# Kernel tuning notes

Measured on AMD Instinct MI355X. Metric: run time of the kernel, lower is better.

Reference implementation:

```python
import jax, jax.numpy as jnp
import numpy as np

B, S, D = 2, 2048, 1024
H, DH = 16, 64
INNER = H * DH  # 1024
FF = 4 * D
WINDOW = 128
EPS = 1e-5
SCALE = DH ** -0.5


def setup_inputs() -> dict:
    key = jax.random.key(0)
    ks = jax.random.split(key, 8)
    s = lambda fan_in: 1.0 / np.sqrt(fan_in)
    return {
        "x": jax.random.normal(ks[0], (B, S, D), dtype=jnp.float32),
        "ln1_g": jnp.ones((D,), jnp.float32),
        "ln1_b": jnp.zeros((D,), jnp.float32),
        "w_qkv": jax.random.uniform(ks[1], (3 * INNER, D), jnp.float32, -s(D), s(D)),
        "w_out": jax.random.uniform(ks[2], (D, INNER), jnp.float32, -s(INNER), s(INNER)),
        "b_out": jnp.zeros((D,), jnp.float32),
        "ln2_g": jnp.ones((D,), jnp.float32),
        "ln2_b": jnp.zeros((D,), jnp.float32),
        "w_ff1": jax.random.uniform(ks[3], (FF, D), jnp.float32, -s(D), s(D)),
        "b_ff1": jnp.zeros((FF,), jnp.float32),
        "w_ff2": jax.random.uniform(ks[4], (D, FF), jnp.float32, -s(FF), s(FF)),
        "b_ff2": jnp.zeros((D,), jnp.float32),
    }


def _layernorm(x, g, b):
    mu = jnp.mean(x, axis=-1, keepdims=True)
    var = jnp.mean(jnp.square(x - mu), axis=-1, keepdims=True)
    return (x - mu) * jax.lax.rsqrt(var + EPS) * g + b


def reference(x, ln1_g, ln1_b, w_qkv, w_out, b_out, ln2_g, ln2_b, w_ff1, b_ff1, w_ff2, b_ff2):
    # --- attention block ---
    residual = x
    h = _layernorm(x, ln1_g, ln1_b)
    qkv = h @ w_qkv.T                             # [B, S, 3*INNER]
    q, k, v = jnp.split(qkv, 3, axis=-1)
    reshape_heads = lambda t: t.reshape(B, S, H, DH).transpose(0, 2, 1, 3)  # [B,H,S,DH]
    q, k, v = map(reshape_heads, (q, k, v))
    q = q * SCALE
    scores = jnp.einsum("bhqd,bhkd->bhqk", q, k)  # dense [B,H,S,S]
    # local sparse pattern: attend iff |i-j| <= window_size
    idx = jnp.arange(S)
    local_mask = jnp.abs(idx[:, None] - idx[None, :]) <= WINDOW  # [S,S] bool
    scores = jnp.where(local_mask[None, None], scores, -jnp.inf)
    attn = jax.nn.softmax(scores, axis=-1)
    attn = jnp.nan_to_num(attn, nan=0.0)
    out = jnp.einsum("bhqk,bhkd->bhqd", attn, v)  # [B,H,S,DH]
    out = out.transpose(0, 2, 1, 3).reshape(B, S, INNER)
    out = out @ w_out.T + b_out                   # dropout inactive (eval)
    x = residual + out
    # --- FFN block ---
    residual = x
    h = _layernorm(x, ln2_g, ln2_b)
    h = jax.nn.gelu(h @ w_ff1.T + b_ff1, approximate=False)
    h = h @ w_ff2.T + b_ff2
    return residual + h
```

## Files before the change

### kernel.cpp

```cpp
#include <hip/hip_runtime.h>
#include <stdint.h>

#define SEQ    2048
#define NB     2
#define DMODEL 1024
#define NHEAD  16
#define HDIM   64
#define FFDIM  4096
#define WIN    128
#define MTOK   (NB*SEQ)

typedef short short8 __attribute__((ext_vector_type(8)));
typedef float f32x4  __attribute__((ext_vector_type(4)));

__device__ __forceinline__ float bf2f(uint16_t h){ return __uint_as_float(((uint32_t)h) << 16); }
__device__ __forceinline__ uint16_t f2bf(float f){
  uint32_t u = __float_as_uint(f);
  u += 0x7fffu + ((u >> 16) & 1u);
  return (uint16_t)(u >> 16);
}

__device__ __forceinline__ float gelu_f(float v){
  float u = 0.7978845608028654f * v * (1.0f + 0.044715f * v * v);
  u = fminf(fmaxf(u, -10.0f), 10.0f);
  const float e = __expf(2.0f * u);
  const float th = (e - 1.0f) / (e + 1.0f);
  return 0.5f * v * (1.0f + th);
}

__device__ __forceinline__ void gl_lds16(const void* g, void* l) {
  __builtin_amdgcn_global_load_lds((const __attribute__((address_space(1))) void*)g,
                                   (__attribute__((address_space(3))) void*)l, 16, 0, 0);
}

__device__ __forceinline__ void BAR() {
  asm volatile("" ::: "memory");
  __builtin_amdgcn_s_barrier();
  asm volatile("" ::: "memory");
}

__global__ __launch_bounds__(256) void cvtln_kernel(
    const float* __restrict__ s0, const float* __restrict__ s1,
    const float* __restrict__ s2, const float* __restrict__ s3,
    uint16_t* __restrict__ d0, uint16_t* __restrict__ d1,
    uint16_t* __restrict__ d2, uint16_t* __restrict__ d3,
    const float* __restrict__ x, const float* __restrict__ g,
    const float* __restrict__ b, uint16_t* __restrict__ y)
{
  __shared__ float red[8];
  const int t = threadIdx.x;
  if (blockIdx.x < 12288) {
    size_t i = (size_t)blockIdx.x * 256 + t;
    const float* s; uint16_t* d; size_t off;
    if      (i <  768*1024) { s = s0; d = d0; off = i; }
    else if (i < 1024*1024) { s = s1; d = d1; off = i -  768*1024; }
    else if (i < 2048*1024) { s = s2; d = d2; off = i - 1024*1024; }
    else                    { s = s3; d = d3; off = i - 2048*1024; }
    const float4 v = ((const float4*)s)[off];
    uint2 o;
    o.x = (uint32_t)f2bf(v.x) | ((uint32_t)f2bf(v.y) << 16);
    o.y = (uint32_t)f2bf(v.z) | ((uint32_t)f2bf(v.w) << 16);
    ((uint2*)d)[off] = o;
  } else {
    const int row = blockIdx.x - 12288;
    const float4 v = ((const float4*)(x + (size_t)row * DMODEL))[t];
    float s1 = v.x + v.y + v.z + v.w;
    float s2 = v.x*v.x + v.y*v.y + v.z*v.z + v.w*v.w;
    #pragma unroll
    for (int off = 32; off; off >>= 1) { s1 += __shfl_xor(s1, off, 64); s2 += __shfl_xor(s2, off, 64); }
    const int w = t >> 6;
    if ((t & 63) == 0) { red[w] = s1; red[4+w] = s2; }
    __syncthreads();
    s1 = red[0]+red[1]+red[2]+red[3];
    s2 = red[4]+red[5]+red[6]+red[7];
    const float mu = s1 * (1.0f/DMODEL);
    const float var = s2 * (1.0f/DMODEL) - mu*mu;
    const float rs = rsqrtf(var + 1e-5f);
    const float4 gv = ((const float4*)g)[t];
    const float4 bv = ((const float4*)b)[t];
    uint2 o;
    o.x = (uint32_t)f2bf((v.x-mu)*rs*gv.x + bv.x) | ((uint32_t)f2bf((v.y-mu)*rs*gv.y + bv.y) << 16);
    o.y = (uint32_t)f2bf((v.z-mu)*rs*gv.z + bv.z) | ((uint32_t)f2bf((v.w-mu)*rs*gv.w + bv.w) << 16);
    ((uint2*)(y + (size_t)row * DMODEL))[t] = o;
  }
}

__global__ __launch_bounds__(256) void ln_kernel(const float* __restrict__ x,
                                                 const float* __restrict__ g,
                                                 const float* __restrict__ b,
                                                 uint16_t* __restrict__ y)
{
  const int row = blockIdx.x;
  const int t = threadIdx.x;
  const float4 v = ((const float4*)(x + (size_t)row * DMODEL))[t];
  float s1 = v.x + v.y + v.z + v.w;
  float s2 = v.x*v.x + v.y*v.y + v.z*v.z + v.w*v.w;
  #pragma unroll
  for (int off = 32; off; off >>= 1) { s1 += __shfl_xor(s1, off, 64); s2 += __shfl_xor(s2, off, 64); }
  __shared__ float red[8];
  const int w = t >> 6;
  if ((t & 63) == 0) { red[w] = s1; red[4+w] = s2; }
  __syncthreads();
  s1 = red[0]+red[1]+red[2]+red[3];
  s2 = red[4]+red[5]+red[6]+red[7];
  const float mu = s1 * (1.0f/DMODEL);
  const float var = s2 * (1.0f/DMODEL) - mu*mu;
  const float rs = rsqrtf(var + 1e-5f);
  const float4 gv = ((const float4*)g)[t];
  const float4 bv = ((const float4*)b)[t];
  uint2 o;
  o.x = (uint32_t)f2bf((v.x-mu)*rs*gv.x + bv.x) | ((uint32_t)f2bf((v.y-mu)*rs*gv.y + bv.y) << 16);
  o.y = (uint32_t)f2bf((v.z-mu)*rs*gv.z + bv.z) | ((uint32_t)f2bf((v.w-mu)*rs*gv.w + bv.w) << 16);
  ((uint2*)(y + (size_t)row * DMODEL))[t] = o;
}

template<int EPI>
__global__ __launch_bounds__(512, 2) void gemm256(
    const uint16_t* __restrict__ A, const uint16_t* __restrict__ Bm,
    const float* __restrict__ bias, uint16_t* __restrict__ C,
    int M, int N, int K)
{
  __shared__ __align__(16) uint16_t L[4 * 16384];
  const int t = threadIdx.x;
  const int l = t & 63;
  const int w = t >> 6;
  const int wm = w >> 2, wn = w & 3;
  const int row0 = blockIdx.y * 256, col0 = blockIdx.x * 256;
  const int mrow = l & 15, kq = l >> 4;
  const int nt = K >> 5;

  f32x4 acc[8][4];
  #pragma unroll
  for (int i = 0; i < 8; ++i)
    #pragma unroll
    for (int j = 0; j < 4; ++j)
      #pragma unroll
      for (int e = 0; e < 4; ++e) acc[i][j][e] = 0.0f;

  const int sr = t >> 2;
  const int kl = (t & 3) ^ ((t >> 3) & 3);
  const uint16_t* aG = A  + (size_t)(row0 + sr) * K + kl * 8;
  const uint16_t* bG = Bm + (size_t)(col0 + sr) * K + kl * 8;
  char* const lds = (char*)L;
  const int soff = t * 16;

  #define STAGE_A(tt_) { char* d_ = lds + ((tt_) & 3) * 32768 + soff; \
      gl_lds16(aG + (tt_) * 32, d_); \
      gl_lds16(aG + (size_t)128 * K + (tt_) * 32, d_ + 8192); }
  #define STAGE_B(tt_) { char* d_ = lds + ((tt_) & 3) * 32768 + 16384 + soff; \
      gl_lds16(bG + (tt_) * 32, d_); \
      gl_lds16(bG + (size_t)128 * K + (tt_) * 32, d_ + 8192); }

  STAGE_A(0); STAGE_B(0);
  STAGE_A(1); STAGE_B(1);
  STAGE_A(2); STAGE_B(2);
  asm volatile("s_waitcnt vmcnt(8)" ::: "memory");
  BAR();

  const int cphys = (kq ^ ((mrow >> 1) & 3)) << 4;

  for (int tt = 0; tt < nt; ++tt) {
    char* const bufA = lds + (tt & 3) * 32768;
    char* const bufB = bufA + 16384;
    short8 bf[4], af[4];
    #pragma unroll
    for (int ni = 0; ni < 4; ++ni)
      bf[ni] = *(const short8*)(bufB + (wn*64 + ni*16 + mrow) * 64 + cphys);
    #pragma unroll
    for (int mi = 0; mi < 4; ++mi)
      af[mi] = *(const short8*)(bufA + (wm*128 + mi*16 + mrow) * 64 + cphys);
    if (tt + 3 < nt) STAGE_A(tt + 3);
    BAR();
    __builtin_amdgcn_s_setprio(1);
    #pragma unroll
    for (int mi = 0; mi < 4; ++mi)
      #pragma unroll
      for (int ni = 0; ni < 4; ++ni)
        acc[mi][ni] = __builtin_amdgcn_mfma_f32_16x16x32_bf16(af[mi], bf[ni], acc[mi][ni], 0, 0, 0);
    __builtin_amdgcn_s_setprio(0);
    BAR();
    #pragma unroll
    for (int mi = 0; mi < 4; ++mi)
      af[mi] = *(const short8*)(bufA + (wm*128 + (mi+4)*16 + mrow) * 64 + cphys);
    if (tt + 3 < nt) {
      STAGE_B(tt + 3);
      asm volatile("s_waitcnt vmcnt(8)" ::: "memory");
    } else if (tt + 3 == nt) {
      asm volatile("s_waitcnt vmcnt(4)" ::: "memory");
    } else if (tt + 2 == nt) {
      asm volatile("s_waitcnt vmcnt(0)" ::: "memory");
    }
    BAR();
    __builtin_amdgcn_s_setprio(1);
    #pragma unroll
    for (int mi = 0; mi < 4; ++mi)
      #pragma unroll
      for (int ni = 0; ni < 4; ++ni)
        acc[mi+4][ni] = __builtin_amdgcn_mfma_f32_16x16x32_bf16(af[mi], bf[ni], acc[mi+4][ni], 0, 0, 0);
    __builtin_amdgcn_s_setprio(0);
    BAR();
  }
  #undef STAGE_A
  #undef STAGE_B

  const int crow = kq * 4;
  float bv[4];
  #pragma unroll
  for (int ni = 0; ni < 4; ++ni)
    bv[ni] = (EPI != 0) ? bias[col0 + wn*64 + ni*16 + mrow] : 0.0f;
  #pragma unroll
  for (int mi = 0; mi < 8; ++mi) {
    #pragma unroll
    for (int r = 0; r < 4; ++r) {
      const int row = row0 + wm*128 + mi*16 + crow + r;
      uint16_t* Cr = C + (size_t)row * N + col0 + wn*64 + mrow;
      #pragma unroll
      for (int ni = 0; ni < 4; ++ni) {
        float v = acc[mi][ni][r] + bv[ni];
        if (EPI == 2) v = gelu_f(v);
        Cr[ni*16] = f2bf(v);
      }
    }
  }
}

__global__ __launch_bounds__(256) void gemm64(
    const uint16_t* __restrict__ A, const uint16_t* __restrict__ Bm,
    const float* __restrict__ bias, const float* __restrict__ res,
    float* __restrict__ out, int M, int N, int K)
{
  __shared__ __align__(16) uint16_t As[64*64];
  __shared__ __align__(16) uint16_t Bs[64*64];
  const int t = threadIdx.x;
  const int l = t & 63;
  const int w = t >> 6;
  const int row0 = blockIdx.y * 64;
  const int col0 = blockIdx.x * 64;
  const int wm = (w >> 1) * 32, wn = (w & 1) * 32;

  f32x4 acc[2][2];
  #pragma unroll
  for (int i = 0; i < 2; ++i)
    #pragma unroll
    for (int j = 0; j < 2; ++j)
      #pragma unroll
      for (int e = 0; e < 4; ++e) acc[i][j][e] = 0.0f;

  const int sr8 = t >> 3;
  const int sg  = (t & 7) ^ (sr8 & 7);
  const uint16_t* aG = A  + (size_t)(row0 + sr8) * K + sg * 8;
  const uint16_t* bG = Bm + (size_t)(col0 + sr8) * K + sg * 8;
  char* aL = (char*)As + t * 16;
  char* bL = (char*)Bs + t * 16;
  const int mrow = l & 15;
  const int kq = l >> 4;

  for (int k0 = 0; k0 < K; k0 += 64) {
    gl_lds16(aG + k0,                    aL);
    gl_lds16(aG + k0 + (size_t)32 * K,   aL + 4096);
    gl_lds16(bG + k0,                    bL);
    gl_lds16(bG + k0 + (size_t)32 * K,   bL + 4096);
    __syncthreads();
    #pragma unroll
    for (int ks = 0; ks < 2; ++ks) {
      const int pa = ((ks*4 + kq) ^ (mrow & 7)) * 16;
      short8 af[2], bfr[2];
      #pragma unroll
      for (int mi = 0; mi < 2; ++mi)
        af[mi] = *(const short8*)((const char*)As + (wm + mi*16 + mrow) * 128 + pa);
      #pragma unroll
      for (int ni = 0; ni < 2; ++ni)
        bfr[ni] = *(const short8*)((const char*)Bs + (wn + ni*16 + mrow) * 128 + pa);
      #pragma unroll
      for (int mi = 0; mi < 2; ++mi)
        #pragma unroll
        for (int ni = 0; ni < 2; ++ni)
          acc[mi][ni] = __builtin_amdgcn_mfma_f32_16x16x32_bf16(af[mi], bfr[ni], acc[mi][ni], 0, 0, 0);
    }
    __syncthreads();
  }

  const int crow = (l >> 4) * 4;
  float bv[2];
  #pragma unroll
  for (int ni = 0; ni < 2; ++ni)
    bv[ni] = bias[col0 + wn + ni*16 + mrow];
  #pragma unroll
  for (int mi = 0; mi < 2; ++mi)
    #pragma unroll
    for (int r = 0; r < 4; ++r) {
      const int row = row0 + wm + mi*16 + crow + r;
      #pragma unroll
      for (int ni = 0; ni < 2; ++ni) {
        const int col = col0 + wn + ni*16 + mrow;
        out[(size_t)row * N + col] = acc[mi][ni][r] + bv[ni] + res[(size_t)row * N + col];
      }
    }
}

#define TQ    32
#define NKT   18
#define NKP   (NKT*16)
#define KSTR  72
#define PSTR  296

__global__ __launch_bounds__(256) void attn_kernel(const uint16_t* __restrict__ qkv,
                                                   uint16_t* __restrict__ out)
{
  __shared__ uint16_t Qs[TQ * KSTR];
  __shared__ uint16_t Ps[TQ * PSTR];
  __shared__ uint16_t KV[NKP * KSTR];
  const int t = threadIdx.x, l = t & 63, w = t >> 6;
  const int b = blockIdx.z, hh = blockIdx.y, q0 = blockIdx.x * TQ;
  const int k0 = (q0 - WIN > 0) ? (q0 - WIN) : 0;
  const int kend_ = q0 + TQ + WIN;
  const int kend = (kend_ < SEQ) ? kend_ : SEQ;
  const int nk = kend - k0;

  {
    const int r = t >> 3, gg = t & 7;
    const uint4 qv = *(const uint4*)(qkv + (size_t)(b*SEQ + q0 + r) * 3072 + hh*64 + gg*8);
    *(uint4*)((char*)Qs + r*(KSTR*2) + gg*16) = qv;
    for (int j = r; j < NKP; j += 32) {
      uint4 kv; kv.x = 0; kv.y = 0; kv.z = 0; kv.w = 0;
      if (j < nk)
        kv = *(const uint4*)(qkv + (size_t)(b*SEQ + k0 + j) * 3072 + 1024 + hh*64 + gg*8);
      *(uint4*)((char*)KV + j*(KSTR*2) + gg*16) = kv;
    }
  }
  __syncthreads();

  if (w < 2) {
    const int rb = w * 16;
    const int mrow = l & 15, q4 = l >> 4;
    const short8 aq0 = *(const short8*)((const char*)Qs + (rb + mrow)*(KSTR*2) + q4*16);
    const short8 aq1 = *(const short8*)((const char*)Qs + (rb + mrow)*(KSTR*2) + 64 + q4*16);
    f32x4 cacc[NKT];
    #pragma unroll
    for (int ct = 0; ct < NKT; ++ct) {
      f32x4 c; c[0]=0.f; c[1]=0.f; c[2]=0.f; c[3]=0.f;
      const short8 b0 = *(const short8*)((const char*)KV + (ct*16 + mrow)*(KSTR*2) + q4*16);
      const short8 b1 = *(const short8*)((const char*)KV + (ct*16 + mrow)*(KSTR*2) + 64 + q4*16);
      c = __builtin_amdgcn_mfma_f32_16x16x32_bf16(aq0, b0, c, 0, 0, 0);
      c = __builtin_amdgcn_mfma_f32_16x16x32_bf16(aq1, b1, c, 0, 0, 0);
      cacc[ct] = c;
    }
    #pragma unroll
    for (int r = 0; r < 4; ++r) {
      const int iq = q0 + rb + q4*4 + r;
      float m = -1e30f;
      #pragma unroll
      for (int ct = 0; ct < NKT; ++ct) {
        const int jj = ct*16 + mrow;
        const int j = k0 + jj;
        const bool ok = (jj < nk) && (j >= iq - WIN) && (j <= iq + WIN);
        const float s = ok ? cacc[ct][r] * 0.125f : -1e30f;
        cacc[ct][r] = s;
        m = fmaxf(m, s);
      }
      m = fmaxf(m, __shfl_xor(m, 1, 64));
      m = fmaxf(m, __shfl_xor(m, 2, 64));
      m = fmaxf(m, __shfl_xor(m, 4, 64));
      m = fmaxf(m, __shfl_xor(m, 8, 64));
      float s = 0.f;
      #pragma unroll
      for (int ct = 0; ct < NKT; ++ct) {
        const float e = __expf(cacc[ct][r] - m);
        cacc[ct][r] = e;
        s += e;
      }
      s += __shfl_xor(s, 1, 64);
      s += __shfl_xor(s, 2, 64);
      s += __shfl_xor(s, 4, 64);
      s += __shfl_xor(s, 8, 64);
      const float rinv = 1.0f / s;
      #pragma unroll
      for (int ct = 0; ct < NKT; ++ct)
        Ps[(rb + q4*4 + r) * PSTR + ct*16 + mrow] = f2bf(cacc[ct][r] * rinv);
    }
  }
  __syncthreads();

  {
    uint16_t* Vt = KV;
    const int gg = t & 7;
    for (int j = t >> 3; j < NKP; j += 32) {
      if (j < nk) {
        const uint4 v = *(const uint4*)(qkv + (size_t)(b*SEQ + k0 + j) * 3072 + 2048 + hh*64 + gg*8);
        uint16_t e[8] = { (uint16_t)(v.x & 0xffff), (uint16_t)(v.x >> 16),
                          (uint16_t)(v.y & 0xffff), (uint16_t)(v.y >> 16),
                          (uint16_t)(v.z & 0xffff), (uint16_t)(v.z >> 16),
                          (uint16_t)(v.w & 0xffff), (uint16_t)(v.w >> 16) };
        #pragma unroll
        for (int dd = 0; dd < 8; ++dd) Vt[(gg*8 + dd) * PSTR + j] = e[dd];
      } else {
        #pragma unroll
        for (int dd = 0; dd < 8; ++dd) Vt[(gg*8 + dd) * PSTR + j] = 0;
      }
    }
  }
  __syncthreads();

  {
    const uint16_t* Vt = KV;
    const int mrow = l & 15, q4 = l >> 4;
    const int rt = w & 1, dt0 = (w >> 1) * 2;
    f32x4 o0, o1;
    #pragma unroll
    for (int e = 0; e < 4; ++e) { o0[e] = 0.f; o1[e] = 0.f; }
    #pragma unroll
    for (int ks = 0; ks < 9; ++ks) {
      const short8 a  = *(const short8*)((const char*)Ps + (rt*16 + mrow)*(PSTR*2) + ks*64 + q4*16);
      const short8 v0 = *(const short8*)((const char*)Vt + ((dt0  )*16 + mrow)*(PSTR*2) + ks*64 + q4*16);
      const short8 v1 = *(const short8*)((const char*)Vt + ((dt0+1)*16 + mrow)*(PSTR*2) + ks*64 + q4*16);
      o0 = __builtin_amdgcn_mfma_f32_16x16x32_bf16(a, v0, o0, 0, 0, 0);
      o1 = __builtin_amdgcn_mfma_f32_16x16x32_bf16(a, v1, o1, 0, 0, 0);
    }
    #pragma unroll
    for (int r = 0; r < 4; ++r) {
      const int iq = q0 + rt*16 + q4*4 + r;
      const size_t rowoff = (size_t)(b*SEQ + iq) * DMODEL + hh*64;
      out[rowoff + (dt0  )*16 + mrow] = f2bf(o0[r]);
      out[rowoff + (dt0+1)*16 + mrow] = f2bf(o1[r]);
    }
  }
}

extern "C" void kernel_launch(void* const* d_in, const int* in_sizes, int n_in,
                              void* d_out, int out_size, void* d_ws, size_t ws_size,
                              hipStream_t stream)
{
  const float* x    = (const float*)d_in[0];
  const float* ln1g = (const float*)d_in[1];
  const float* ln1b = (const float*)d_in[2];
  const float* wqkv = (const float*)d_in[3];
  const float* wout = (const float*)d_in[4];
  const float* bout = (const float*)d_in[5];
  const float* ln2g = (const float*)d_in[6];
  const float* ln2b = (const float*)d_in[7];
  const float* wff1 = (const float*)d_in[8];
  const float* bff1 = (const float*)d_in[9];
  const float* wff2 = (const float*)d_in[10];
  const float* bff2 = (const float*)d_in[11];
  float* out = (float*)d_out;

  char* ws = (char*)d_ws;
  const size_t MB = (size_t)1 << 20;
  uint16_t* Wqkv = (uint16_t*)(ws);
  uint16_t* Wout = (uint16_t*)(ws +  6*MB);
  uint16_t* Wff1 = (uint16_t*)(ws +  8*MB);
  uint16_t* Wff2 = (uint16_t*)(ws + 16*MB);
  uint16_t* QKV  = (uint16_t*)(ws + 24*MB);
  uint16_t* H1   = (uint16_t*)(ws + 48*MB);
  uint16_t* AT   = H1;
  float*    X2f  = (float*)   (ws + 56*MB);
  uint16_t* H2   = (uint16_t*)(ws + 72*MB);
  uint16_t* FF1  = (uint16_t*)(ws + 24*MB);

  cvtln_kernel<<<16384, 256, 0, stream>>>(wqkv, wout, wff1, wff2,
                                          Wqkv, Wout, Wff1, Wff2,
                                          x, ln1g, ln1b, H1);
  gemm256<0><<<dim3(3072/256, MTOK/256), 512, 0, stream>>>(H1, Wqkv, nullptr, QKV, MTOK, 3072, DMODEL);
  attn_kernel<<<dim3(SEQ/TQ, NHEAD, NB), 256, 0, stream>>>(QKV, AT);
  gemm64<<<dim3(DMODEL/64, MTOK/64), 256, 0, stream>>>(AT, Wout, bout, x, X2f, MTOK, DMODEL, DMODEL);
  ln_kernel<<<MTOK, 256, 0, stream>>>(X2f, ln2g, ln2b, H2);
  gemm256<2><<<dim3(FFDIM/256, MTOK/256), 512, 0, stream>>>(H2, Wff1, bff1, FF1, MTOK, FFDIM, DMODEL);
  gemm64<<<dim3(DMODEL/64, MTOK/64), 256, 0, stream>>>(FF1, Wff2, bff2, X2f, out, MTOK, DMODEL, FFDIM);
}
```

Before: 331.7 us.

## Replace gemm64 with pipelined 128x128 GEMM and overlap V staging in attention

Replaces the 64x64 single-buffered residual GEMM with a 128x128, 512-thread kernel. It uses a 4-deep LDS ring of direct global-to-LDS loads, explicit vmcnt waits, and s_setprio around the MFMA bursts, to hide load latency and cut per-tile overhead. The attention kernel now prefetches V into registers while Q/K are staged, and moves the V-transpose onto the two idle waves so it runs alongside the softmax. It also swizzles the transposed V layout to reduce LDS bank conflicts. The costs are extra registers, 128KB of LDS per block for the GEMM (which limits occupancy), and a subtle wait-count schedule.

After: 314.8 us. 5.1% less time.

```diff
diff --git a/kernel.cpp b/kernel.cpp
--- a/kernel.cpp
+++ b/kernel.cpp
@@ -224,77 +224,116 @@
   }
 }
 
-__global__ __launch_bounds__(256) void gemm64(
+__global__ __launch_bounds__(512, 2) void gemm128r(
     const uint16_t* __restrict__ A, const uint16_t* __restrict__ Bm,
     const float* __restrict__ bias, const float* __restrict__ res,
     float* __restrict__ out, int M, int N, int K)
 {
-  __shared__ __align__(16) uint16_t As[64*64];
-  __shared__ __align__(16) uint16_t Bs[64*64];
+  __shared__ __align__(16) uint16_t L[4 * 16384];
   const int t = threadIdx.x;
   const int l = t & 63;
   const int w = t >> 6;
-  const int row0 = blockIdx.y * 64;
-  const int col0 = blockIdx.x * 64;
-  const int wm = (w >> 1) * 32, wn = (w & 1) * 32;
-
-  f32x4 acc[2][2];
-  #pragma unroll
-  for (int i = 0; i < 2; ++i)
+  const int wm = w >> 2, wn = w & 3;
+  const int row0 = blockIdx.x * 128, col0 = blockIdx.y * 128;
+  const int mrow = l & 15, kq = l >> 4;
+  const int nt = K >> 6;
+
+  f32x4 acc[4][2];
+  #pragma unroll
+  for (int i = 0; i < 4; ++i)
     #pragma unroll
     for (int j = 0; j < 2; ++j)
       #pragma unroll
       for (int e = 0; e < 4; ++e) acc[i][j][e] = 0.0f;
 
-  const int sr8 = t >> 3;
-  const int sg  = (t & 7) ^ (sr8 & 7);
-  const uint16_t* aG = A  + (size_t)(row0 + sr8) * K + sg * 8;
-  const uint16_t* bG = Bm + (size_t)(col0 + sr8) * K + sg * 8;
-  char* aL = (char*)As + t * 16;
-  char* bL = (char*)Bs + t * 16;
-  const int mrow = l & 15;
-  const int kq = l >> 4;
-
-  for (int k0 = 0; k0 < K; k0 += 64) {
-    gl_lds16(aG + k0,                    aL);
-    gl_lds16(aG + k0 + (size_t)32 * K,   aL + 4096);
-    gl_lds16(bG + k0,                    bL);
-    gl_lds16(bG + k0 + (size_t)32 * K,   bL + 4096);
-    __syncthreads();
-    #pragma unroll
-    for (int ks = 0; ks < 2; ++ks) {
-      const int pa = ((ks*4 + kq) ^ (mrow & 7)) * 16;
-      short8 af[2], bfr[2];
-      #pragma unroll
-      for (int mi = 0; mi < 2; ++mi)
-        af[mi] = *(const short8*)((const char*)As + (wm + mi*16 + mrow) * 128 + pa);
+  const int sr = t >> 3;
+  const int kl = (t & 7) ^ (sr & 7);
+  const uint16_t* aG = A  + (size_t)(row0 + sr) * K + kl * 8;
+  const uint16_t* bG = Bm + (size_t)(col0 + sr) * K + kl * 8;
+  char* const lds = (char*)L;
+  const int soff = t * 16;
+
+  #define STAGE_A(tt_) { char* d_ = lds + ((tt_) & 3) * 32768 + soff; \
+      gl_lds16(aG + (tt_) * 64, d_); \
+      gl_lds16(aG + (size_t)64 * K + (tt_) * 64, d_ + 8192); }
+  #define STAGE_B(tt_) { char* d_ = lds + ((tt_) & 3) * 32768 + 16384 + soff; \
+      gl_lds16(bG + (tt_) * 64, d_); \
+      gl_lds16(bG + (size_t)64 * K + (tt_) * 64, d_ + 8192); }
+
+  STAGE_A(0); STAGE_B(0);
+  STAGE_A(1); STAGE_B(1);
+  STAGE_A(2); STAGE_B(2);
+  asm volatile("s_waitcnt vmcnt(8)" ::: "memory");
+  BAR();
+
+  for (int tt = 0; tt < nt; ++tt) {
+    char* const bufA = lds + (tt & 3) * 32768;
+    char* const bufB = bufA + 16384;
+    {
+      const int pa = (kq ^ (mrow & 7)) * 16;
+      short8 af[4], bf[2];
       #pragma unroll
       for (int ni = 0; ni < 2; ++ni)
-        bfr[ni] = *(const short8*)((const char*)Bs + (wn + ni*16 + mrow) * 128 + pa);
-      #pragma unroll
-      for (int mi = 0; mi < 2; ++mi)
+        bf[ni] = *(const short8*)(bufB + (wn*32 + ni*16 + mrow) * 128 + pa);
+      #pragma unroll
+      for (int mi = 0; mi < 4; ++mi)
+        af[mi] = *(const short8*)(bufA + (wm*64 + mi*16 + mrow) * 128 + pa);
+      if (tt + 3 < nt) STAGE_A(tt + 3);
+      BAR();
+      __builtin_amdgcn_s_setprio(1);
+      #pragma unroll
+      for (int mi = 0; mi < 4; ++mi)
         #pragma unroll
         for (int ni = 0; ni < 2; ++ni)
-          acc[mi][ni] = __builtin_amdgcn_mfma_f32_16x16x32_bf16(af[mi], bfr[ni], acc[mi][ni], 0, 0, 0);
-    }
-    __syncthreads();
-  }
-
-  const int crow = (l >> 4) * 4;
+          acc[mi][ni] = __builtin_amdgcn_mfma_f32_16x16x32_bf16(af[mi], bf[ni], acc[mi][ni], 0, 0, 0);
+      __builtin_amdgcn_s_setprio(0);
+      BAR();
+    }
+    {
+      const int pa = ((4 + kq) ^ (mrow & 7)) * 16;
+      short8 af[4], bf[2];
+      #pragma unroll
+      for (int ni = 0; ni < 2; ++ni)
+        bf[ni] = *(const short8*)(bufB + (wn*32 + ni*16 + mrow) * 128 + pa);
+      #pragma unroll
+      for (int mi = 0; mi < 4; ++mi)
+        af[mi] = *(const short8*)(bufA + (wm*64 + mi*16 + mrow) * 128 + pa);
+      if (tt + 3 < nt) {
+        STAGE_B(tt + 3);
+        asm volatile("s_waitcnt vmcnt(8)" ::: "memory");
+      } else if (tt + 3 == nt) {
+        asm volatile("s_waitcnt vmcnt(4)" ::: "memory");
+      } else if (tt + 2 == nt) {
+        asm volatile("s_waitcnt vmcnt(0)" ::: "memory");
+      }
+      BAR();
+      __builtin_amdgcn_s_setprio(1);
+      #pragma unroll
+      for (int mi = 0; mi < 4; ++mi)
+        #pragma unroll
+        for (int ni = 0; ni < 2; ++ni)
+          acc[mi][ni] = __builtin_amdgcn_mfma_f32_16x16x32_bf16(af[mi], bf[ni], acc[mi][ni], 0, 0, 0);
+      __builtin_amdgcn_s_setprio(0);
+      BAR();
+    }
+  }
+  #undef STAGE_A
+  #undef STAGE_B
+
+  const int crow = kq * 4;
   float bv[2];
   #pragma unroll
   for (int ni = 0; ni < 2; ++ni)
-    bv[ni] = bias[col0 + wn + ni*16 + mrow];
-  #pragma unroll
-  for (int mi = 0; mi < 2; ++mi)
+    bv[ni] = bias[col0 + wn*32 + ni*16 + mrow];
+  #pragma unroll
+  for (int mi = 0; mi < 4; ++mi)
     #pragma unroll
     for (int r = 0; r < 4; ++r) {
-      const int row = row0 + wm + mi*16 + crow + r;
-      #pragma unroll
-      for (int ni = 0; ni < 2; ++ni) {
-        const int col = col0 + wn + ni*16 + mrow;
-        out[(size_t)row * N + col] = acc[mi][ni][r] + bv[ni] + res[(size_t)row * N + col];
-      }
+      const int row = row0 + wm*64 + mi*16 + crow + r;
+      const size_t base = (size_t)row * N + col0 + wn*32 + mrow;
+      #pragma unroll
+      for (int ni = 0; ni < 2; ++ni)
+        out[base + ni*16] = acc[mi][ni][r] + bv[ni] + res[base + ni*16];
     }
 }
 
@@ -303,6 +342,9 @@
 #define NKP   (NKT*16)
 #define KSTR  72
 #define PSTR  296
+#define VSTR  320
+
+__device__ __forceinline__ int vt_swz(int d){ return (d >> 3) ^ ((d & 3) << 1); }
 
 __global__ __launch_bounds__(256) void attn_kernel(const uint16_t* __restrict__ qkv,
                                                    uint16_t* __restrict__ out)
@@ -328,14 +370,28 @@
       *(uint4*)((char*)KV + j*(KSTR*2) + gg*16) = kv;
     }
   }
+
+  const int tt2 = t & 127;
+  const int jl = tt2 >> 3, gg2 = tt2 & 7;
+  uint4 va[9];
+  if (w >= 2) {
+    #pragma unroll
+    for (int i = 0; i < 9; ++i) {
+      uint4 z; z.x = 0; z.y = 0; z.z = 0; z.w = 0;
+      const int j = jl + 16*i;
+      va[i] = (j < nk)
+        ? *(const uint4*)(qkv + (size_t)(b*SEQ + k0 + j) * 3072 + 2048 + hh*64 + gg2*8)
+        : z;
+    }
+  }
   __syncthreads();
 
+  const int mrow = l & 15, q4 = l >> 4;
+  f32x4 cacc[NKT];
   if (w < 2) {
     const int rb = w * 16;
-    const int mrow = l & 15, q4 = l >> 4;
     const short8 aq0 = *(const short8*)((const char*)Qs + (rb + mrow)*(KSTR*2) + q4*16);
     const short8 aq1 = *(const short8*)((const char*)Qs + (rb + mrow)*(KSTR*2) + 64 + q4*16);
-    f32x4 cacc[NKT];
     #pragma unroll
     for (int ct = 0; ct < NKT; ++ct) {
       f32x4 c; c[0]=0.f; c[1]=0.f; c[2]=0.f; c[3]=0.f;
@@ -345,6 +401,11 @@
       c = __builtin_amdgcn_mfma_f32_16x16x32_bf16(aq1, b1, c, 0, 0, 0);
       cacc[ct] = c;
     }
+  }
+  __syncthreads();
+
+  if (w < 2) {
+    const int rb = w * 16;
     #pragma unroll
     for (int r = 0; r < 4; ++r) {
       const int iq = q0 + rb + q4*4 + r;
@@ -378,24 +439,30 @@
       for (int ct = 0; ct < NKT; ++ct)
         Ps[(rb + q4*4 + r) * PSTR + ct*16 + mrow] = f2bf(cacc[ct][r] * rinv);
     }
-  }
-  __syncthreads();
-
-  {
+  } else {
     uint16_t* Vt = KV;
-    const int gg = t & 7;
-    for (int j = t >> 3; j < NKP; j += 32) {
-      if (j < nk) {
-        const uint4 v = *(const uint4*)(qkv + (size_t)(b*SEQ + k0 + j) * 3072 + 2048 + hh*64 + gg*8);
-        uint16_t e[8] = { (uint16_t)(v.x & 0xffff), (uint16_t)(v.x >> 16),
-                          (uint16_t)(v.y & 0xffff), (uint16_t)(v.y >> 16),
-                          (uint16_t)(v.z & 0xffff), (uint16_t)(v.z >> 16),
-                          (uint16_t)(v.w & 0xffff), (uint16_t)(v.w >> 16) };
-        #pragma unroll
-        for (int dd = 0; dd < 8; ++dd) Vt[(gg*8 + dd) * PSTR + j] = e[dd];
-      } else {
-        #pragma unroll
-        for (int dd = 0; dd < 8; ++dd) Vt[(gg*8 + dd) * PSTR + j] = 0;
+    uint4 vb[9];
+    #pragma unroll
+    for (int i = 0; i < 9; ++i) {
+      uint4 z; z.x = 0; z.y = 0; z.z = 0; z.w = 0;
+      const int j = jl + 16*(i+9);
+      vb[i] = (j < nk)
+        ? *(const uint4*)(qkv + (size_t)(b*SEQ + k0 + j) * 3072 + 2048 + hh*64 + gg2*8)
+        : z;
+    }
+    #pragma unroll
+    for (int i = 0; i < 18; ++i) {
+      const uint4 v = (i < 9) ? va[i] : vb[i-9];
+      const int j = jl + 16*i;
+      const uint16_t e[8] = { (uint16_t)(v.x & 0xffff), (uint16_t)(v.x >> 16),
+                              (uint16_t)(v.y & 0xffff), (uint16_t)(v.y >> 16),
+                              (uint16_t)(v.z & 0xffff), (uint16_t)(v.z >> 16),
+                              (uint16_t)(v.w & 0xffff), (uint16_t)(v.w >> 16) };
+      #pragma unroll
+      for (int dd = 0; dd < 8; ++dd) {
+        const int dr = gg2*8 + dd;
+        const int coff = (((j >> 3) ^ vt_swz(dr)) << 4) + ((j & 7) << 1);
+        *(uint16_t*)((char*)Vt + dr*(VSTR*2) + coff) = e[dd];
       }
     }
   }
@@ -403,16 +470,18 @@
 
   {
     const uint16_t* Vt = KV;
-    const int mrow = l & 15, q4 = l >> 4;
     const int rt = w & 1, dt0 = (w >> 1) * 2;
     f32x4 o0, o1;
     #pragma unroll
     for (int e = 0; e < 4; ++e) { o0[e] = 0.f; o1[e] = 0.f; }
+    const int d0 = (dt0  )*16 + mrow;
+    const int d1 = (dt0+1)*16 + mrow;
+    const int sw0 = vt_swz(d0), sw1 = vt_swz(d1);
     #pragma unroll
     for (int ks = 0; ks < 9; ++ks) {
       const short8 a  = *(const short8*)((const char*)Ps + (rt*16 + mrow)*(PSTR*2) + ks*64 + q4*16);
-      const short8 v0 = *(const short8*)((const char*)Vt + ((dt0  )*16 + mrow)*(PSTR*2) + ks*64 + q4*16);
-      const short8 v1 = *(const short8*)((const char*)Vt + ((dt0+1)*16 + mrow)*(PSTR*2) + ks*64 + q4*16);
+      const short8 v0 = *(const short8*)((const char*)Vt + d0*(VSTR*2) + (((ks*4 + q4) ^ sw0) << 4));
+      const short8 v1 = *(const short8*)((const char*)Vt + d1*(VSTR*2) + (((ks*4 + q4) ^ sw1) << 4));
       o0 = __builtin_amdgcn_mfma_f32_16x16x32_bf16(a, v0, o0, 0, 0, 0);
       o1 = __builtin_amdgcn_mfma_f32_16x16x32_bf16(a, v1, o1, 0, 0, 0);
     }
@@ -462,8 +531,8 @@
                                           x, ln1g, ln1b, H1);
   gemm256<0><<<dim3(3072/256, MTOK/256), 512, 0, stream>>>(H1, Wqkv, nullptr, QKV, MTOK, 3072, DMODEL);
   attn_kernel<<<dim3(SEQ/TQ, NHEAD, NB), 256, 0, stream>>>(QKV, AT);
-  gemm64<<<dim3(DMODEL/64, MTOK/64), 256, 0, stream>>>(AT, Wout, bout, x, X2f, MTOK, DMODEL, DMODEL);
+  gemm128r<<<dim3(MTOK/128, DMODEL/128), 512, 0, stream>>>(AT, Wout, bout, x, X2f, MTOK, DMODEL, DMODEL);
   ln_kernel<<<MTOK, 256, 0, stream>>>(X2f, ln2g, ln2b, H2);
   gemm256<2><<<dim3(FFDIM/256, MTOK/256), 512, 0, stream>>>(H2, Wff1, bff1, FF1, MTOK, FFDIM, DMODEL);
-  gemm64<<<dim3(DMODEL/64, MTOK/64), 256, 0, stream>>>(FF1, Wff2, bff2, X2f, out, MTOK, DMODEL, FFDIM);
-}
+  gemm128r<<<dim3(MTOK/128, DMODEL/128), 512, 0, stream>>>(FF1, Wff2, bff2, X2f, out, MTOK, DMODEL, FFDIM);
+}
```
